# Kernel optimization log

Measured on AMD Instinct MI355X. Metric: run time of the kernel, lower is better.

## Reference

```python
import jax, jax.numpy as jnp
import numpy as np

E, D, H, T = 16, 1024, 4096, 8192  # num_expert, d_model, d_hidden (4h), total tokens


def setup_inputs() -> dict:
    key = jax.random.key(0)
    k0, k1, k2, k3, k4 = jax.random.split(key, 5)
    inp = jax.random.normal(k0, (T, D), dtype=jnp.float32)
    # FMoELinear init: kaiming-uniform-like, bound = 1/sqrt(fan_in)
    s1 = 1.0 / np.sqrt(D)
    s2 = 1.0 / np.sqrt(H)
    w1 = jax.random.uniform(k1, (E, H, D), jnp.float32, -s1, s1)  # htoh4 weight [E, out, in]
    b1 = jax.random.uniform(k2, (E, H), jnp.float32, -s1, s1)
    w2 = jax.random.uniform(k3, (E, D, H), jnp.float32, -s2, s2)  # h4toh weight
    b2 = jax.random.uniform(k4, (E, D), jnp.float32, -s2, s2)
    fwd_expert_count = jnp.full((E,), T // E, dtype=jnp.int32)  # tokens per expert (sums to T)
    return dict(inp=inp, w1=w1, b1=b1, w2=w2, b2=b2, fwd_expert_count=fwd_expert_count)


def reference(inp, w1, b1, w2, b2, fwd_expert_count):
    # Grouped GEMM: tokens are sorted by expert; segment e gets expert e's FFN.
    counts = np.asarray(fwd_expert_count)          # static per-expert row counts
    offs = np.concatenate([[0], np.cumsum(counts)])
    outs = []
    for e in range(counts.shape[0]):               # loop over fixed small expert set
        seg = inp[offs[e]:offs[e + 1]]             # [n_e, D]
        h = seg @ w1[e].T + b1[e]                  # htoh4: [n_e, H]
        h = jax.nn.gelu(h, approximate=False)      # torch F.gelu default (exact)
        outs.append(h @ w2[e].T + b2[e])           # h4toh: [n_e, D]
    return jnp.concatenate(outs, axis=0)           # [T, D]
```

## Files before the change

### kernel.cpp

```cpp
#include <hip/hip_runtime.h>
#include <hip/hip_bf16.h>

typedef float f32x4 __attribute__((ext_vector_type(4)));
typedef int   i32x4 __attribute__((ext_vector_type(4)));
typedef __bf16 bf16x8 __attribute__((ext_vector_type(8)));
typedef unsigned short u16;
typedef unsigned short u16x4 __attribute__((ext_vector_type(4)));
typedef unsigned short u16x8 __attribute__((ext_vector_type(8)));

#define BM 128
#define BN 128
#define BK 32
#define NT 256
#define MAXE 32

__device__ __forceinline__ u16 f2bf(float f) {
  __bf16 h = (__bf16)f;
  return __builtin_bit_cast(u16, h);
}

typedef const __attribute__((address_space(1))) void GAS;
typedef __attribute__((address_space(3))) void LAS;
__device__ __forceinline__ void gl_lds16(const void* g, void* l) {
  __builtin_amdgcn_global_load_lds((GAS*)g, (LAS*)l, 16, 0, 0);
}

__global__ __launch_bounds__(256)
void cvt_bf16(const float* __restrict__ in, u16* __restrict__ out, int n8) {
  int i = blockIdx.x * 256 + threadIdx.x;
  if (i < n8) {
    f32x4 a = *(const f32x4*)(in + (long long)i * 8);
    f32x4 b = *(const f32x4*)(in + (long long)i * 8 + 4);
    u16x8 r = { f2bf(a[0]), f2bf(a[1]), f2bf(a[2]), f2bf(a[3]),
                f2bf(b[0]), f2bf(b[1]), f2bf(b[2]), f2bf(b[3]) };
    *(u16x8*)(out + (long long)i * 8) = r;
  }
}

__device__ __forceinline__ int expert_lookup(const int* counts, int E, int bm,
                                             int mt_in, int& row0, int& cnt, int& mt) {
  int cs[MAXE];
#pragma unroll
  for (int j = 0; j < MAXE / 4; ++j) {
    if (j * 4 + 3 < E) *(i32x4*)&cs[j * 4] = *(const i32x4*)(counts + j * 4);
    else {
#pragma unroll
      for (int q = 0; q < 4; ++q) cs[j*4+q] = (j*4+q < E) ? counts[j*4+q] : 0;
    }
  }
  int e = -1; row0 = 0; cnt = 0; mt = mt_in;
#pragma unroll
  for (int i = 0; i < MAXE; ++i) {
    if (i < E && e < 0) {
      int ntl = (cs[i] + bm - 1) / bm;
      if (mt < ntl) { e = i; cnt = cs[i]; }
      else { mt -= ntl; row0 += cs[i]; }
    }
  }
  return e;
}

__global__ __launch_bounds__(NT)
void ffn_gemm1(const u16* __restrict__ Ain, const float* __restrict__ Bw,
               const float* __restrict__ bias, u16* __restrict__ Out,
               const int* __restrict__ counts, int E, int T, int N, int K)
{
  int row0, cnt, mt;
  int e = expert_lookup(counts, E, BM, blockIdx.y, row0, cnt, mt);
  if (e < 0) return;
  int valid = cnt - mt * BM; if (valid > BM) valid = BM;
  row0 += mt * BM;
  const int n0 = blockIdx.x * BN;

  const float* Be = Bw + (long long)e * N * K;
  const float* be = bias + (long long)e * N;

  __shared__ u16  As[2][BM * BK];
  __shared__ float Bs[2][BN * BK];

  const int t = threadIdx.x;
  const int lane = t & 63;
  const int w = t >> 6, wr = w >> 1, wc = w & 1;
  const int NKT = K / BK;

  int aSrc[2], aDst[2];
#pragma unroll
  for (int s = 0; s < 2; ++s) {
    int rb = (s * 4 + w) * 16;
    int r = rb + (lane >> 2);
    int gr = row0 + r; if (gr > T - 1) gr = T - 1;
    aSrc[s] = gr * K + ((lane & 3) << 3);
    aDst[s] = rb * BK;
  }
  int bSrc[4], bDst[4];
#pragma unroll
  for (int s = 0; s < 4; ++s) {
    int rb = (s * 4 + w) * 8;
    int r = rb + (lane >> 3);
    bSrc[s] = (n0 + r) * K + (((lane & 7) ^ (r & 7)) << 2);
    bDst[s] = rb * BK;
  }

  auto stage = [&](int buf, int kt) {
    const int k0 = kt * BK;
#pragma unroll
    for (int s = 0; s < 2; ++s) gl_lds16(Ain + aSrc[s] + k0, &As[buf][aDst[s]]);
#pragma unroll
    for (int s = 0; s < 4; ++s) gl_lds16(Be + bSrc[s] + k0, &Bs[buf][bDst[s]]);
  };

  const int rl = lane & 15, kg = lane >> 4;
  int aoff[4], boff[4];
#pragma unroll
  for (int mf = 0; mf < 4; ++mf) {
    int R = wr * 64 + mf * 16 + rl;
    aoff[mf] = R * BK + kg * 8;
  }
#pragma unroll
  for (int nf = 0; nf < 4; ++nf) {
    int R = wc * 64 + nf * 16 + rl;
    int go = (2 * kg) ^ (R & 7);
    boff[nf] = R * BK + go * 4;
  }

  f32x4 acc[4][4];
#pragma unroll
  for (int i = 0; i < 4; ++i)
#pragma unroll
    for (int j = 0; j < 4; ++j) acc[i][j] = (f32x4){0.f, 0.f, 0.f, 0.f};

  stage(0, 0);
  __syncthreads();

  for (int kt = 0; kt < NKT; ++kt) {
    const int cur = kt & 1;
    if (kt + 1 < NKT) stage(cur ^ 1, kt + 1);

    bf16x8 af[4], bfr[4];
#pragma unroll
    for (int mf = 0; mf < 4; ++mf)
      af[mf] = __builtin_bit_cast(bf16x8, *(const u16x8*)&As[cur][aoff[mf]]);
#pragma unroll
    for (int nf = 0; nf < 4; ++nf) {
      f32x4 lo = *(const f32x4*)&Bs[cur][boff[nf]];
      f32x4 hi = *(const f32x4*)&Bs[cur][boff[nf] ^ 4];
      u16x8 r = { f2bf(lo[0]), f2bf(lo[1]), f2bf(lo[2]), f2bf(lo[3]),
                  f2bf(hi[0]), f2bf(hi[1]), f2bf(hi[2]), f2bf(hi[3]) };
      bfr[nf] = __builtin_bit_cast(bf16x8, r);
    }

    __builtin_amdgcn_s_setprio(1);
#pragma unroll
    for (int mf = 0; mf < 4; ++mf)
#pragma unroll
      for (int nf = 0; nf < 4; ++nf)
        acc[mf][nf] = __builtin_amdgcn_mfma_f32_16x16x32_bf16(af[mf], bfr[nf], acc[mf][nf], 0, 0, 0);
    __builtin_amdgcn_s_setprio(0);

    __syncthreads();
  }

  const int cl = lane & 15, rg = lane >> 4;
#pragma unroll
  for (int mf = 0; mf < 4; ++mf) {
#pragma unroll
    for (int nf = 0; nf < 4; ++nf) {
      int gcol = n0 + wc * 64 + nf * 16 + cl;
      float bv = be[gcol];
#pragma unroll
      for (int r = 0; r < 4; ++r) {
        int lrow = wr * 64 + mf * 16 + rg * 4 + r;
        if (lrow < valid) {
          float v = acc[mf][nf][r] + bv;
          v = 0.5f * v * (1.0f + erff(v * 0.70710678118654752f));
          Out[(long long)(row0 + lrow) * N + gcol] = f2bf(v);
        }
      }
    }
  }
}

template<bool DO_GELU, bool OUT_BF16>
__global__ __launch_bounds__(NT)
void ffn_gemm(const u16* __restrict__ Ain, const float* __restrict__ Bw,
              const float* __restrict__ bias, void* __restrict__ Out,
              const int* __restrict__ counts, int E, int T, int N, int K)
{
  int row0, cnt, mt;
  int e = expert_lookup(counts, E, BM, blockIdx.y, row0, cnt, mt);
  if (e < 0) return;
  int valid = cnt - mt * BM; if (valid > BM) valid = BM;
  row0 += mt * BM;
  const int n0 = blockIdx.x * BN;

  const float* Be = Bw + (long long)e * N * K;
  const float* be = bias + (long long)e * N;

  __shared__ u16 As[2][BM][BK];
  __shared__ u16 Bs[2][BN][BK];

  const int t = threadIdx.x;
  const int lane = t & 63;
  const int w = t >> 6, wr = w >> 1, wc = w & 1;
  const int NKT = K / BK;

  long long offA[2];
#pragma unroll
  for (int i = 0; i < 2; ++i) {
    int c = i * NT + t;
    int row = c >> 2, col = (c & 3) << 3;
    int gr = row0 + row; if (gr > T - 1) gr = T - 1;
    offA[i] = (long long)gr * K + col;
  }
  long long offB[4];
#pragma unroll
  for (int i = 0; i < 4; ++i) {
    int c = i * NT + t;
    offB[i] = (long long)(n0 + (c >> 3)) * K + ((c & 7) << 2);
  }

  f32x4 acc[4][4];
#pragma unroll
  for (int i = 0; i < 4; ++i)
#pragma unroll
    for (int j = 0; j < 4; ++j) acc[i][j] = (f32x4){0.f, 0.f, 0.f, 0.f};

  u16x8 rAu[2]; float rB[16];

  auto load_g = [&](int kt) {
    const int k0 = kt * BK;
#pragma unroll
    for (int i = 0; i < 2; ++i)
      rAu[i] = *(const u16x8*)(Ain + offA[i] + k0);
#pragma unroll
    for (int i = 0; i < 4; ++i) {
      f32x4 v = *(const f32x4*)(Be + offB[i] + k0);
      rB[i*4+0] = v[0]; rB[i*4+1] = v[1]; rB[i*4+2] = v[2]; rB[i*4+3] = v[3];
    }
  };

  auto store_tile = [&](int buf) {
#pragma unroll
    for (int i = 0; i < 2; ++i) {
      int c = i * NT + t;
      int row = c >> 2, col = (c & 3) << 3;
      int kg2 = (col >> 3) ^ ((row >> 1) & 3);
      *(u16x8*)&As[buf][row][kg2 * 8] = rAu[i];
    }
#pragma unroll
    for (int i = 0; i < 4; ++i) {
      int c = i * NT + t;
      int row = c >> 3, col = (c & 7) << 2;
      int kg2 = (col >> 3) ^ ((row >> 1) & 3);
      int off = kg2 * 8 + ((col >> 2) & 1) * 4;
      u16x4 pk = { f2bf(rB[i*4+0]), f2bf(rB[i*4+1]), f2bf(rB[i*4+2]), f2bf(rB[i*4+3]) };
      *(u16x4*)&Bs[buf][row][off] = pk;
    }
  };

  load_g(0);
  store_tile(0);
  load_g(1);
  __syncthreads();

  const int rl = lane & 15;
  const int kgf = (lane >> 4) ^ ((rl >> 1) & 3);

  for (int kt = 0; kt < NKT; ++kt) {
    const int cur = kt & 1;

    bf16x8 af[4], bfr[4];
#pragma unroll
    for (int mf = 0; mf < 4; ++mf)
      af[mf] = __builtin_bit_cast(bf16x8, *(const u16x8*)&As[cur][wr*64 + mf*16 + rl][kgf*8]);
#pragma unroll
    for (int nf = 0; nf < 4; ++nf)
      bfr[nf] = __builtin_bit_cast(bf16x8, *(const u16x8*)&Bs[cur][wc*64 + nf*16 + rl][kgf*8]);

    if (kt + 1 < NKT) store_tile(cur ^ 1);
    if (kt + 2 < NKT) load_g(kt + 2);

#pragma unroll
    for (int mf = 0; mf < 4; ++mf)
#pragma unroll
      for (int nf = 0; nf < 4; ++nf)
        acc[mf][nf] = __builtin_amdgcn_mfma_f32_16x16x32_bf16(af[mf], bfr[nf], acc[mf][nf], 0, 0, 0);

    if (kt + 1 < NKT) __syncthreads();
  }

  const int cl = lane & 15, rg = lane >> 4;
#pragma unroll
  for (int mf = 0; mf < 4; ++mf) {
#pragma unroll
    for (int nf = 0; nf < 4; ++nf) {
      int gcol = n0 + wc*64 + nf*16 + cl;
      float bv = be[gcol];
#pragma unroll
      for (int r = 0; r < 4; ++r) {
        int lrow = wr*64 + mf*16 + rg*4 + r;
        if (lrow < valid) {
          float v = acc[mf][nf][r] + bv;
          if constexpr (DO_GELU)
            v = 0.5f * v * (1.0f + erff(v * 0.70710678118654752f));
          long long idx = (long long)(row0 + lrow) * N + gcol;
          if constexpr (OUT_BF16) ((u16*)Out)[idx] = f2bf(v);
          else                    ((float*)Out)[idx] = v;
        }
      }
    }
  }
}

extern "C" void kernel_launch(void* const* d_in, const int* in_sizes, int n_in,
                              void* d_out, int out_size, void* d_ws, size_t ws_size,
                              hipStream_t stream) {
  const float* inp = (const float*)d_in[0];
  const float* w1  = (const float*)d_in[1];
  const float* b1  = (const float*)d_in[2];
  const float* w2  = (const float*)d_in[3];
  const float* b2  = (const float*)d_in[4];
  const int* cnts  = (const int*)d_in[5];

  const int E = in_sizes[5];
  const int H = in_sizes[2] / E;
  const int D = in_sizes[4] / E;
  const int T = in_sizes[0] / D;

  u16* hbuf = (u16*)d_ws;
  u16* ibuf = (u16*)((char*)d_ws + (size_t)T * H * 2);

  const int n8 = (T * D) / 8;
  cvt_bf16<<<dim3((n8 + 255) / 256), dim3(256), 0, stream>>>(inp, ibuf, n8);

  const int tiles = T / BM + E;

  dim3 g1(H / BN, tiles);
  ffn_gemm1<<<g1, dim3(NT), 0, stream>>>(ibuf, w1, b1, hbuf, cnts, E, T, H, D);

  dim3 g2(D / BN, tiles);
  ffn_gemm<false, false><<<g2, dim3(NT), 0, stream>>>(
      hbuf, w2, b2, d_out, cnts, E, T, D, H);
}
```

Before: 346.0 us.

## Retile first expert GEMM to 512x128 with register-staged bf16 weight conversion

Rewrites the first grouped GEMM to use 512-row by 128-column tiles with 512 threads, so each fp32 weight tile is loaded and converted once per 512 tokens rather than per 128. Weights are converted to bf16 in registers before being stored to LDS, which halves the LDS footprint for B and removes per-iteration conversion in the MFMA loop. Direct global-to-LDS loads are replaced by a register prefetch pipeline two tiles ahead, with an XOR swizzle on LDS. The larger tile uses more registers and reduces the number of blocks. With 512 tokens per expert, each expert maps to exactly one M tile.

```diff
diff --git a/kernel.cpp b/kernel.cpp
--- a/kernel.cpp
+++ b/kernel.cpp
@@ -8,21 +8,11 @@
 typedef unsigned short u16x4 __attribute__((ext_vector_type(4)));
 typedef unsigned short u16x8 __attribute__((ext_vector_type(8)));
 
-#define BM 128
-#define BN 128
-#define BK 32
-#define NT 256
 #define MAXE 32
 
 __device__ __forceinline__ u16 f2bf(float f) {
   __bf16 h = (__bf16)f;
   return __builtin_bit_cast(u16, h);
-}
-
-typedef const __attribute__((address_space(1))) void GAS;
-typedef __attribute__((address_space(3))) void LAS;
-__device__ __forceinline__ void gl_lds16(const void* g, void* l) {
-  __builtin_amdgcn_global_load_lds((GAS*)g, (LAS*)l, 16, 0, 0);
 }
 
 __global__ __launch_bounds__(256)
@@ -60,116 +50,132 @@
   return e;
 }
 
-__global__ __launch_bounds__(NT)
+#define B1M 512
+#define B1N 128
+#define B1K 32
+#define N1T 512
+
+__global__ __launch_bounds__(N1T, 2)
 void ffn_gemm1(const u16* __restrict__ Ain, const float* __restrict__ Bw,
                const float* __restrict__ bias, u16* __restrict__ Out,
                const int* __restrict__ counts, int E, int T, int N, int K)
 {
   int row0, cnt, mt;
-  int e = expert_lookup(counts, E, BM, blockIdx.y, row0, cnt, mt);
+  int e = expert_lookup(counts, E, B1M, blockIdx.y, row0, cnt, mt);
   if (e < 0) return;
-  int valid = cnt - mt * BM; if (valid > BM) valid = BM;
-  row0 += mt * BM;
-  const int n0 = blockIdx.x * BN;
+  int valid = cnt - mt * B1M; if (valid > B1M) valid = B1M;
+  row0 += mt * B1M;
+  const int n0 = blockIdx.x * B1N;
 
   const float* Be = Bw + (long long)e * N * K;
   const float* be = bias + (long long)e * N;
 
-  __shared__ u16  As[2][BM * BK];
-  __shared__ float Bs[2][BN * BK];
+  __shared__ u16 As[2][B1M][B1K];
+  __shared__ u16 Bs[2][B1N][B1K];
 
   const int t = threadIdx.x;
   const int lane = t & 63;
   const int w = t >> 6, wr = w >> 1, wc = w & 1;
-  const int NKT = K / BK;
-
-  int aSrc[2], aDst[2];
-#pragma unroll
-  for (int s = 0; s < 2; ++s) {
-    int rb = (s * 4 + w) * 16;
-    int r = rb + (lane >> 2);
-    int gr = row0 + r; if (gr > T - 1) gr = T - 1;
-    aSrc[s] = gr * K + ((lane & 3) << 3);
-    aDst[s] = rb * BK;
-  }
-  int bSrc[4], bDst[4];
-#pragma unroll
-  for (int s = 0; s < 4; ++s) {
-    int rb = (s * 4 + w) * 8;
-    int r = rb + (lane >> 3);
-    bSrc[s] = (n0 + r) * K + (((lane & 7) ^ (r & 7)) << 2);
-    bDst[s] = rb * BK;
-  }
-
-  auto stage = [&](int buf, int kt) {
-    const int k0 = kt * BK;
-#pragma unroll
-    for (int s = 0; s < 2; ++s) gl_lds16(Ain + aSrc[s] + k0, &As[buf][aDst[s]]);
-#pragma unroll
-    for (int s = 0; s < 4; ++s) gl_lds16(Be + bSrc[s] + k0, &Bs[buf][bDst[s]]);
+  const int NKT = K / B1K;
+
+  long long offA[4];
+  int aRow[4], aCol[4];
+#pragma unroll
+  for (int i = 0; i < 4; ++i) {
+    int c = i * N1T + t;
+    aRow[i] = c >> 2; aCol[i] = (c & 3) << 3;
+    int gr = row0 + aRow[i]; if (gr > T - 1) gr = T - 1;
+    offA[i] = (long long)gr * K + aCol[i];
+  }
+  long long offB[2];
+  int bRow[2], bCol[2];
+#pragma unroll
+  for (int i = 0; i < 2; ++i) {
+    int c = i * N1T + t;
+    bRow[i] = c >> 3; bCol[i] = (c & 7) << 2;
+    offB[i] = (long long)(n0 + bRow[i]) * K + bCol[i];
+  }
+
+  f32x4 acc[8][4];
+#pragma unroll
+  for (int i = 0; i < 8; ++i)
+#pragma unroll
+    for (int j = 0; j < 4; ++j) acc[i][j] = (f32x4){0.f, 0.f, 0.f, 0.f};
+
+  u16x8 rAu[4]; float rB[8];
+
+  auto load_g = [&](int kt) {
+    const int k0 = kt * B1K;
+#pragma unroll
+    for (int i = 0; i < 4; ++i)
+      rAu[i] = *(const u16x8*)(Ain + offA[i] + k0);
+#pragma unroll
+    for (int i = 0; i < 2; ++i) {
+      f32x4 v = *(const f32x4*)(Be + offB[i] + k0);
+      rB[i*4+0] = v[0]; rB[i*4+1] = v[1]; rB[i*4+2] = v[2]; rB[i*4+3] = v[3];
+    }
   };
 
-  const int rl = lane & 15, kg = lane >> 4;
-  int aoff[4], boff[4];
-#pragma unroll
-  for (int mf = 0; mf < 4; ++mf) {
-    int R = wr * 64 + mf * 16 + rl;
-    aoff[mf] = R * BK + kg * 8;
-  }
-#pragma unroll
-  for (int nf = 0; nf < 4; ++nf) {
-    int R = wc * 64 + nf * 16 + rl;
-    int go = (2 * kg) ^ (R & 7);
-    boff[nf] = R * BK + go * 4;
-  }
-
-  f32x4 acc[4][4];
-#pragma unroll
-  for (int i = 0; i < 4; ++i)
-#pragma unroll
-    for (int j = 0; j < 4; ++j) acc[i][j] = (f32x4){0.f, 0.f, 0.f, 0.f};
-
-  stage(0, 0);
+  auto store_tile = [&](int buf) {
+#pragma unroll
+    for (int i = 0; i < 4; ++i) {
+      int row = aRow[i], col = aCol[i];
+      int kg = (col >> 3) ^ ((row >> 1) & 3);
+      *(u16x8*)&As[buf][row][kg * 8] = rAu[i];
+    }
+#pragma unroll
+    for (int i = 0; i < 2; ++i) {
+      int row = bRow[i], col = bCol[i];
+      int kg = (col >> 3) ^ ((row >> 1) & 3);
+      int off = kg * 8 + ((col >> 2) & 1) * 4;
+      u16x4 pk = { f2bf(rB[i*4+0]), f2bf(rB[i*4+1]), f2bf(rB[i*4+2]), f2bf(rB[i*4+3]) };
+      *(u16x4*)&Bs[buf][row][off] = pk;
+    }
+  };
+
+  load_g(0);
+  store_tile(0);
+  load_g(1);
   __syncthreads();
+
+  const int rl = lane & 15;
+  const int kgf = (lane >> 4) ^ ((rl >> 1) & 3);
 
   for (int kt = 0; kt < NKT; ++kt) {
     const int cur = kt & 1;
-    if (kt + 1 < NKT) stage(cur ^ 1, kt + 1);
-
-    bf16x8 af[4], bfr[4];
-#pragma unroll
-    for (int mf = 0; mf < 4; ++mf)
-      af[mf] = __builtin_bit_cast(bf16x8, *(const u16x8*)&As[cur][aoff[mf]]);
-#pragma unroll
-    for (int nf = 0; nf < 4; ++nf) {
-      f32x4 lo = *(const f32x4*)&Bs[cur][boff[nf]];
-      f32x4 hi = *(const f32x4*)&Bs[cur][boff[nf] ^ 4];
-      u16x8 r = { f2bf(lo[0]), f2bf(lo[1]), f2bf(lo[2]), f2bf(lo[3]),
-                  f2bf(hi[0]), f2bf(hi[1]), f2bf(hi[2]), f2bf(hi[3]) };
-      bfr[nf] = __builtin_bit_cast(bf16x8, r);
-    }
+
+    bf16x8 af[8], bfr[4];
+#pragma unroll
+    for (int nf = 0; nf < 4; ++nf)
+      bfr[nf] = __builtin_bit_cast(bf16x8, *(const u16x8*)&Bs[cur][wc*64 + nf*16 + rl][kgf*8]);
+#pragma unroll
+    for (int mf = 0; mf < 8; ++mf)
+      af[mf] = __builtin_bit_cast(bf16x8, *(const u16x8*)&As[cur][wr*128 + mf*16 + rl][kgf*8]);
+
+    if (kt + 1 < NKT) store_tile(cur ^ 1);
+    if (kt + 2 < NKT) load_g(kt + 2);
 
     __builtin_amdgcn_s_setprio(1);
 #pragma unroll
-    for (int mf = 0; mf < 4; ++mf)
+    for (int mf = 0; mf < 8; ++mf)
 #pragma unroll
       for (int nf = 0; nf < 4; ++nf)
         acc[mf][nf] = __builtin_amdgcn_mfma_f32_16x16x32_bf16(af[mf], bfr[nf], acc[mf][nf], 0, 0, 0);
     __builtin_amdgcn_s_setprio(0);
 
-    __syncthreads();
+    if (kt + 1 < NKT) __syncthreads();
   }
 
   const int cl = lane & 15, rg = lane >> 4;
 #pragma unroll
-  for (int mf = 0; mf < 4; ++mf) {
-#pragma unroll
-    for (int nf = 0; nf < 4; ++nf) {
-      int gcol = n0 + wc * 64 + nf * 16 + cl;
-      float bv = be[gcol];
+  for (int nf = 0; nf < 4; ++nf) {
+    int gcol = n0 + wc * 64 + nf * 16 + cl;
+    float bv = be[gcol];
+#pragma unroll
+    for (int mf = 0; mf < 8; ++mf) {
 #pragma unroll
       for (int r = 0; r < 4; ++r) {
-        int lrow = wr * 64 + mf * 16 + rg * 4 + r;
+        int lrow = wr * 128 + mf * 16 + rg * 4 + r;
         if (lrow < valid) {
           float v = acc[mf][nf][r] + bv;
           v = 0.5f * v * (1.0f + erff(v * 0.70710678118654752f));
@@ -179,6 +185,11 @@
     }
   }
 }
+
+#define BM 128
+#define BN 128
+#define BK 32
+#define NT 256
 
 template<bool DO_GELU, bool OUT_BF16>
 __global__ __launch_bounds__(NT)
@@ -333,12 +344,12 @@
   const int n8 = (T * D) / 8;
   cvt_bf16<<<dim3((n8 + 255) / 256), dim3(256), 0, stream>>>(inp, ibuf, n8);
 
-  const int tiles = T / BM + E;
-
-  dim3 g1(H / BN, tiles);
-  ffn_gemm1<<<g1, dim3(NT), 0, stream>>>(ibuf, w1, b1, hbuf, cnts, E, T, H, D);
-
-  dim3 g2(D / BN, tiles);
+  const int tiles1 = T / B1M + E;
+  dim3 g1(H / B1N, tiles1);
+  ffn_gemm1<<<g1, dim3(N1T), 0, stream>>>(ibuf, w1, b1, hbuf, cnts, E, T, H, D);
+
+  const int tiles2 = T / BM + E;
+  dim3 g2(D / BN, tiles2);
   ffn_gemm<false, false><<<g2, dim3(NT), 0, stream>>>(
       hbuf, w2, b2, d_out, cnts, E, T, D, H);
 }
```

Result: slower. 360.7 us (+4.3%).

## Triple-buffer gemm1 loads with vmcnt waits and rotate K start per block

Applied to the files above, without the earlier changes.

Moves the first GEMM from double to triple buffering in LDS, so loads are issued two k-tiles ahead. The full __syncthreads is replaced by explicit s_waitcnt vmcnt counts plus an s_barrier, letting one tile's loads stay in flight while the current tile is computed. It also rotates each block's starting k-tile by blockIdx.y so concurrent blocks read different regions of the weight matrix, which is meant to spread memory-channel traffic. The third buffer raises LDS use per block (about 72KB), which may reduce occupancy.

```diff
diff --git a/kernel.cpp b/kernel.cpp
--- a/kernel.cpp
+++ b/kernel.cpp
@@ -8,10 +8,6 @@
 typedef unsigned short u16x4 __attribute__((ext_vector_type(4)));
 typedef unsigned short u16x8 __attribute__((ext_vector_type(8)));
 
-#define BM 128
-#define BN 128
-#define BK 32
-#define NT 256
 #define MAXE 32
 
 __device__ __forceinline__ u16 f2bf(float f) {
@@ -60,28 +56,32 @@
   return e;
 }
 
-__global__ __launch_bounds__(NT)
+__global__ __launch_bounds__(256)
 void ffn_gemm1(const u16* __restrict__ Ain, const float* __restrict__ Bw,
                const float* __restrict__ bias, u16* __restrict__ Out,
                const int* __restrict__ counts, int E, int T, int N, int K)
 {
+#define G1BM 128
+#define G1BN 128
+#define G1BK 32
   int row0, cnt, mt;
-  int e = expert_lookup(counts, E, BM, blockIdx.y, row0, cnt, mt);
+  int e = expert_lookup(counts, E, G1BM, blockIdx.y, row0, cnt, mt);
   if (e < 0) return;
-  int valid = cnt - mt * BM; if (valid > BM) valid = BM;
-  row0 += mt * BM;
-  const int n0 = blockIdx.x * BN;
+  int valid = cnt - mt * G1BM; if (valid > G1BM) valid = G1BM;
+  row0 += mt * G1BM;
+  const int n0 = blockIdx.x * G1BN;
 
   const float* Be = Bw + (long long)e * N * K;
   const float* be = bias + (long long)e * N;
 
-  __shared__ u16  As[2][BM * BK];
-  __shared__ float Bs[2][BN * BK];
+  __shared__ u16  As[3][G1BM * G1BK];
+  __shared__ float Bs[3][G1BN * G1BK];
 
   const int t = threadIdx.x;
   const int lane = t & 63;
   const int w = t >> 6, wr = w >> 1, wc = w & 1;
-  const int NKT = K / BK;
+  const int NKT = K / G1BK;
+  const int rot = (blockIdx.y & 3) * 8;
 
   int aSrc[2], aDst[2];
 #pragma unroll
@@ -90,7 +90,7 @@
     int r = rb + (lane >> 2);
     int gr = row0 + r; if (gr > T - 1) gr = T - 1;
     aSrc[s] = gr * K + ((lane & 3) << 3);
-    aDst[s] = rb * BK;
+    aDst[s] = rb * G1BK;
   }
   int bSrc[4], bDst[4];
 #pragma unroll
@@ -98,11 +98,11 @@
     int rb = (s * 4 + w) * 8;
     int r = rb + (lane >> 3);
     bSrc[s] = (n0 + r) * K + (((lane & 7) ^ (r & 7)) << 2);
-    bDst[s] = rb * BK;
-  }
-
-  auto stage = [&](int buf, int kt) {
-    const int k0 = kt * BK;
+    bDst[s] = rb * G1BK;
+  }
+
+  auto stage = [&](int buf, int ktp) {
+    const int k0 = ktp * G1BK;
 #pragma unroll
     for (int s = 0; s < 2; ++s) gl_lds16(Ain + aSrc[s] + k0, &As[buf][aDst[s]]);
 #pragma unroll
@@ -114,13 +114,13 @@
 #pragma unroll
   for (int mf = 0; mf < 4; ++mf) {
     int R = wr * 64 + mf * 16 + rl;
-    aoff[mf] = R * BK + kg * 8;
+    aoff[mf] = R * G1BK + kg * 8;
   }
 #pragma unroll
   for (int nf = 0; nf < 4; ++nf) {
     int R = wc * 64 + nf * 16 + rl;
     int go = (2 * kg) ^ (R & 7);
-    boff[nf] = R * BK + go * 4;
+    boff[nf] = R * G1BK + go * 4;
   }
 
   f32x4 acc[4][4];
@@ -129,12 +129,15 @@
 #pragma unroll
     for (int j = 0; j < 4; ++j) acc[i][j] = (f32x4){0.f, 0.f, 0.f, 0.f};
 
-  stage(0, 0);
-  __syncthreads();
+  stage(0, rot % NKT);
+  stage(1, (1 + rot) % NKT);
+  asm volatile("s_waitcnt vmcnt(6)" ::: "memory");
+  __builtin_amdgcn_s_barrier();
+  __builtin_amdgcn_sched_barrier(0);
 
   for (int kt = 0; kt < NKT; ++kt) {
-    const int cur = kt & 1;
-    if (kt + 1 < NKT) stage(cur ^ 1, kt + 1);
+    const int cur = kt % 3;
+    if (kt + 2 < NKT) stage((kt + 2) % 3, (kt + 2 + rot) % NKT);
 
     bf16x8 af[4], bfr[4];
 #pragma unroll
@@ -157,7 +160,12 @@
         acc[mf][nf] = __builtin_amdgcn_mfma_f32_16x16x32_bf16(af[mf], bfr[nf], acc[mf][nf], 0, 0, 0);
     __builtin_amdgcn_s_setprio(0);
 
-    __syncthreads();
+    if (kt + 1 < NKT) {
+      if (kt + 2 < NKT) asm volatile("s_waitcnt vmcnt(6)" ::: "memory");
+      else              asm volatile("s_waitcnt vmcnt(0)" ::: "memory");
+      __builtin_amdgcn_s_barrier();
+      __builtin_amdgcn_sched_barrier(0);
+    }
   }
 
   const int cl = lane & 15, rg = lane >> 4;
@@ -179,6 +187,11 @@
     }
   }
 }
+
+#define BM 128
+#define BN 128
+#define BK 32
+#define NT 256
 
 template<bool DO_GELU, bool OUT_BF16>
 __global__ __launch_bounds__(NT)
```

Result: slower. 404.4 us (+16.9%).
